# Optimization experiments

Measured on AMD Instinct MI355X. Metric: run time of the kernel, lower is better.

## Reference

```python
import jax, jax.numpy as jnp
import numpy as np

H = 512
S = 65  # 64 board cells + appended constant 1


def _heads(y, wk, wq, wv):
    # y: [H, S]; wk/wq/wv: [3, H, H] -> atts: [3, S, H]
    def one(wk_i, wq_i, wv_i):
        k = wk_i @ y            # [H, S]
        q = wq_i @ y            # [H, S]
        v = wv_i @ y            # [H, S]
        sm = jax.nn.softmax(k.T @ q, axis=1)  # [S, S], softmax over dim=1
        return sm @ v.T         # [S, H]
    return jax.vmap(one)(wk, wq, wv)


def setup_inputs() -> dict:
    key = jax.random.key(0)
    ks = jax.random.split(key, 10)
    r = lambda k, s: jax.random.normal(k, s, dtype=jnp.float32)
    return {
        "inputs": r(ks[0], (1, 64)),
        "embedding": r(ks[1], (H, S)),
        "wq": r(ks[2], (3, 3, H, H)),
        "wk": r(ks[3], (3, 3, H, H)),
        "wv": r(ks[4], (3, 3, H, H)),
        "linear1": r(ks[5], (3 * H, H)),
        "linear2": r(ks[6], (3 * H, H)),
        "linear3": r(ks[7], (3 * H, 2 * H)),
        "linear4": r(ks[8], (2 * H, H)),
        "linear5": r(ks[9], (H, 64)),
    }


def reference(inputs, embedding, wq, wk, wv, linear1, linear2, linear3, linear4, linear5):
    x = jnp.concatenate([inputs[0], jnp.ones((1,), inputs.dtype)])  # [S]
    y = embedding * x  # [H, S] (broadcast over rows)

    # Layer 1 (3 heads)
    a1 = _heads(y, wk[0], wq[0], wv[0])  # [3, S, H]
    y = jax.nn.relu(jnp.concatenate([a1[0], a1[1], a1[2]], axis=1) @ linear1).T  # [H, S]

    # Layer 2 -- NOTE: original code cats att11, att12, att23 (a bug we preserve)
    a2 = _heads(y, wk[1], wq[1], wv[1])
    y = jax.nn.relu(jnp.concatenate([a1[0], a1[1], a2[2]], axis=1) @ linear2).T  # [H, S]

    # Layer 3 -- NOTE: original code cats att11, att12, att33 (preserved)
    a3 = _heads(y, wk[2], wq[2], wv[2])
    y = jax.nn.relu(jnp.concatenate([a1[0], a1[1], a3[2]], axis=1) @ linear3)[64]  # [2H]

    # dropout p=0.1 -> identity in eval mode
    y = jnp.tanh(y @ linear4)  # [H]
    score = y @ linear5        # [64]
    return score[None, :]      # [1, 64]
```

## Files before the change

kernel.cpp:

```cpp
#include <hip/hip_runtime.h>
#include <hip/hip_bf16.h>
#include <math.h>

#define H 512
#define S 65
#define SP 80
#define HS (H * S)
#define PHS (H * SP)
#define KS3 24
#define KS4 16


__global__ void scale_embed_kernel(const float* __restrict__ inp,
                                   const float* __restrict__ emb,
                                   float* __restrict__ yT) {
    int i = blockIdx.x * blockDim.x + threadIdx.x;
    if (i < PHS) {
        int s = i / H;
        int h = i % H;
        float v = 0.0f;
        if (s < S) {
            float x = (s == 64) ? 1.0f : inp[s];
            v = emb[h * S + s] * x;
        }
        yT[i] = v;
    }
}

__global__ void __launch_bounds__(256, 2)
kqv_gemm_tiled(const float* __restrict__ wq,
               const float* __restrict__ wk,
               const float* __restrict__ wv,
               int layer, int head0,
               const float* __restrict__ yT,
               float* __restrict__ part) {
    int slot  = blockIdx.z;
    int which = blockIdx.y;
    int mat = layer * 3 + head0 + slot;
    const float* W = (which == 0 ? wk : (which == 1 ? wq : wv)) + (size_t)mat * H * H;

    int n0   = (blockIdx.x & 7) * 64;
    int kidx = blockIdx.x >> 3;

    __shared__ float Wt[64 * 64];
    __shared__ float As[SP * 64];

    int t  = threadIdx.x;
    int nq = t & 15;
    int g  = t >> 4;

    float4 acc[5];
#pragma unroll
    for (int r = 0; r < 5; ++r) acc[r] = make_float4(0.f, 0.f, 0.f, 0.f);

    for (int ch = 0; ch < 4; ++ch) {
        int kc0 = kidx * 256 + ch * 64;

#pragma unroll
        for (int c = 0; c < 4; ++c) {
            int f = c * 256 + t;
            int wn  = f >> 4;
            int kf4 = f & 15;
            float4 w4 = *(const float4*)(W + (size_t)(n0 + wn) * H + kc0 + 4 * kf4);
            int sw = ((wn >> 2) ^ (kf4 & 7));
            int base = (4 * kf4) * 64 + 4 * sw + (wn & 3);
            Wt[base      ] = w4.x;
            Wt[base +  64] = w4.y;
            Wt[base + 128] = w4.z;
            Wt[base + 192] = w4.w;
        }
#pragma unroll
        for (int c = 0; c < 5; ++c) {
            int f = c * 256 + t;
            int as  = f >> 4;
            int kf4 = f & 15;
            *(float4*)(&As[as * 64 + 4 * kf4]) =
                *(const float4*)(yT + (size_t)as * H + kc0 + 4 * kf4);
        }
        __syncthreads();

#pragma unroll
        for (int k4 = 0; k4 < 16; ++k4) {
            int swc = 4 * (nq ^ (k4 & 7));
            float4 w0 = *(const float4*)(&Wt[(4 * k4 + 0) * 64 + swc]);
            float4 w1 = *(const float4*)(&Wt[(4 * k4 + 1) * 64 + swc]);
            float4 w2 = *(const float4*)(&Wt[(4 * k4 + 2) * 64 + swc]);
            float4 w3 = *(const float4*)(&Wt[(4 * k4 + 3) * 64 + swc]);
#pragma unroll
            for (int r = 0; r < 5; ++r) {
                float4 a = *(const float4*)(&As[(g + 16 * r) * 64 + 4 * k4]);
                acc[r].x = fmaf(a.x, w0.x, acc[r].x);
                acc[r].y = fmaf(a.x, w0.y, acc[r].y);
                acc[r].z = fmaf(a.x, w0.z, acc[r].z);
                acc[r].w = fmaf(a.x, w0.w, acc[r].w);
                acc[r].x = fmaf(a.y, w1.x, acc[r].x);
                acc[r].y = fmaf(a.y, w1.y, acc[r].y);
                acc[r].z = fmaf(a.y, w1.z, acc[r].z);
                acc[r].w = fmaf(a.y, w1.w, acc[r].w);
                acc[r].x = fmaf(a.z, w2.x, acc[r].x);
                acc[r].y = fmaf(a.z, w2.y, acc[r].y);
                acc[r].z = fmaf(a.z, w2.z, acc[r].z);
                acc[r].w = fmaf(a.z, w2.w, acc[r].w);
                acc[r].x = fmaf(a.w, w3.x, acc[r].x);
                acc[r].y = fmaf(a.w, w3.y, acc[r].y);
                acc[r].z = fmaf(a.w, w3.z, acc[r].z);
                acc[r].w = fmaf(a.w, w3.w, acc[r].w);
            }
        }
        __syncthreads();
    }

    float* P = part + (size_t)((slot * 3 + which) * 2 + kidx) * PHS;
#pragma unroll
    for (int r = 0; r < 5; ++r) {
        *(float4*)(P + (size_t)(g + 16 * r) * H + n0 + 4 * nq) = acc[r];
    }
}

__global__ void kqv_combine_kernel(const float* __restrict__ part,
                                   float* __restrict__ kT,
                                   float* __restrict__ qT,
                                   float* __restrict__ vT) {
    int slot  = blockIdx.z;
    int which = blockIdx.y;
    int i = blockIdx.x * 256 + threadIdx.x;
    float* out = (which == 0 ? kT : (which == 1 ? qT : vT)) + (size_t)slot * PHS;
    const float* P = part + (size_t)((slot * 3 + which) * 2) * PHS;
    out[i] = P[i] + P[PHS + i];
}

__global__ void attn_kernel(const float* __restrict__ kT,
                            const float* __restrict__ qT,
                            const float* __restrict__ vT,
                            float* __restrict__ att, int a_offset) {
    int a = blockIdx.x + a_offset;
    int slot = blockIdx.y;
    int tid = threadIdx.x;

    const float* kk = kT + (size_t)slot * PHS;
    const float* qq = qT + (size_t)slot * PHS;
    const float* vv = vT + (size_t)slot * PHS;
    float* ao = att + (size_t)slot * S * H;

    __shared__ float sm[S];
    __shared__ float p[S];

    const float4* ka = (const float4*)(kk + (size_t)a * H);
    for (int b = tid; b < S; b += 64) {
        const float4* qb = (const float4*)(qq + (size_t)b * H);
        float4 c0 = {0,0,0,0}, c1 = {0,0,0,0}, c2 = {0,0,0,0}, c3 = {0,0,0,0};
        for (int t = 0; t < H / 4; t += 4) {
            float4 k0 = ka[t+0], k1 = ka[t+1], k2 = ka[t+2], k3 = ka[t+3];
            float4 q0 = qb[t+0], q1 = qb[t+1], q2 = qb[t+2], q3 = qb[t+3];
            c0.x = fmaf(k0.x, q0.x, c0.x); c0.y = fmaf(k0.y, q0.y, c0.y);
            c0.z = fmaf(k0.z, q0.z, c0.z); c0.w = fmaf(k0.w, q0.w, c0.w);
            c1.x = fmaf(k1.x, q1.x, c1.x); c1.y = fmaf(k1.y, q1.y, c1.y);
            c1.z = fmaf(k1.z, q1.z, c1.z); c1.w = fmaf(k1.w, q1.w, c1.w);
            c2.x = fmaf(k2.x, q2.x, c2.x); c2.y = fmaf(k2.y, q2.y, c2.y);
            c2.z = fmaf(k2.z, q2.z, c2.z); c2.w = fmaf(k2.w, q2.w, c2.w);
            c3.x = fmaf(k3.x, q3.x, c3.x); c3.y = fmaf(k3.y, q3.y, c3.y);
            c3.z = fmaf(k3.z, q3.z, c3.z); c3.w = fmaf(k3.w, q3.w, c3.w);
        }
        sm[b] = ((c0.x + c0.y) + (c0.z + c0.w)) + ((c1.x + c1.y) + (c1.z + c1.w))
              + ((c2.x + c2.y) + (c2.z + c2.w)) + ((c3.x + c3.y) + (c3.z + c3.w));
    }
    __syncthreads();

    float maxv = -INFINITY;
    for (int i = 0; i < S; ++i) maxv = fmaxf(maxv, sm[i]);
    float sum = 0.0f;
    for (int i = 0; i < S; ++i) sum += expf(sm[i] - maxv);
    float inv = 1.0f / sum;
    for (int b = tid; b < S; b += 64) {
        p[b] = expf(sm[b] - maxv) * inv;
    }
    __syncthreads();

    for (int hh = tid; hh < H; hh += 64) {
        float a0 = 0.f, a1 = 0.f, a2 = 0.f, a3 = 0.f;
        for (int b = 0; b < 64; b += 4) {
            a0 = fmaf(p[b + 0], vv[(b + 0) * H + hh], a0);
            a1 = fmaf(p[b + 1], vv[(b + 1) * H + hh], a1);
            a2 = fmaf(p[b + 2], vv[(b + 2) * H + hh], a2);
            a3 = fmaf(p[b + 3], vv[(b + 3) * H + hh], a3);
        }
        a0 = fmaf(p[64], vv[64 * H + hh], a0);
        ao[(size_t)a * H + hh] = (a0 + a1) + (a2 + a3);
    }
}

__global__ void linear_partial_kernel(const float* __restrict__ attA,
                                      const float* __restrict__ attB,
                                      const float* __restrict__ attC,
                                      const float* __restrict__ lin,
                                      float* __restrict__ part) {
    int seg = blockIdx.y;
    const float* att = (seg < 2) ? attA : (seg < 4 ? attB : attC);
    int i = blockIdx.x * blockDim.x + threadIdx.x;
    if (i >= HS) return;
    int s = i / H;
    int h = i % H;

    const float* row = att + (size_t)s * H + (seg & 1) * 256;
    const float* L = lin + (size_t)(seg * 256) * H + h;

    float a0 = 0.f, a1 = 0.f, a2 = 0.f, a3 = 0.f;
    for (int j = 0; j < 256; j += 4) {
        a0 = fmaf(row[j + 0], L[(size_t)(j + 0) * H], a0);
        a1 = fmaf(row[j + 1], L[(size_t)(j + 1) * H], a1);
        a2 = fmaf(row[j + 2], L[(size_t)(j + 2) * H], a2);
        a3 = fmaf(row[j + 3], L[(size_t)(j + 3) * H], a3);
    }
    part[(size_t)seg * HS + i] = (a0 + a1) + (a2 + a3);
}

__global__ void combine_relu_kernel(const float* __restrict__ part,
                                    float* __restrict__ yT) {
    int i = blockIdx.x * blockDim.x + threadIdx.x;
    if (i >= HS) return;
    float s = part[i] + part[HS + i] + part[2 * HS + i]
            + part[3 * HS + i] + part[4 * HS + i] + part[5 * HS + i];
    yT[i] = fmaxf(s, 0.0f);
}

__global__ void lin3_partial_kernel(const float* __restrict__ attA,
                                    const float* __restrict__ attB,
                                    const float* __restrict__ attC,
                                    const float* __restrict__ lin3,
                                    float* __restrict__ tpart) {
    int j2 = blockIdx.x * 256 + threadIdx.x;
    int ks = blockIdx.y;
    const float* row = (ks < 8) ? (attA + (size_t)64 * H)
                     : (ks < 16 ? (attB + (size_t)64 * H)
                                : (attC + (size_t)64 * H));
    int j0 = (ks & 7) * 64;
    int jbase = ks * 64;

    float a0 = 0.f, a1 = 0.f, a2 = 0.f, a3 = 0.f;
    for (int j = 0; j < 64; j += 4) {
        a0 = fmaf(row[j0 + j + 0], lin3[(size_t)(jbase + j + 0) * 1024 + j2], a0);
        a1 = fmaf(row[j0 + j + 1], lin3[(size_t)(jbase + j + 1) * 1024 + j2], a1);
        a2 = fmaf(row[j0 + j + 2], lin3[(size_t)(jbase + j + 2) * 1024 + j2], a2);
        a3 = fmaf(row[j0 + j + 3], lin3[(size_t)(jbase + j + 3) * 1024 + j2], a3);
    }
    tpart[ks * 1024 + j2] = (a0 + a1) + (a2 + a3);
}

__global__ void lin4_partial_kernel(const float* __restrict__ tpart,
                                    const float* __restrict__ lin4,
                                    float* __restrict__ upart) {
    __shared__ float tl[64];
    int hh = blockIdx.x * 256 + threadIdx.x;
    int ks = blockIdx.y;
    int j2base = ks * 64;

    if (threadIdx.x < 64) {
        int j2 = j2base + threadIdx.x;
        float s = 0.f;
#pragma unroll
        for (int p = 0; p < KS3; ++p) s += tpart[p * 1024 + j2];
        tl[threadIdx.x] = fmaxf(s, 0.f);
    }
    __syncthreads();

    float a0 = 0.f, a1 = 0.f, a2 = 0.f, a3 = 0.f;
    for (int j = 0; j < 64; j += 4) {
        a0 = fmaf(tl[j + 0], lin4[(size_t)(j2base + j + 0) * H + hh], a0);
        a1 = fmaf(tl[j + 1], lin4[(size_t)(j2base + j + 1) * H + hh], a1);
        a2 = fmaf(tl[j + 2], lin4[(size_t)(j2base + j + 2) * H + hh], a2);
        a3 = fmaf(tl[j + 3], lin4[(size_t)(j2base + j + 3) * H + hh], a3);
    }
    upart[ks * H + hh] = (a0 + a1) + (a2 + a3);
}

__global__ void final_out_kernel(const float* __restrict__ upart,
                                 const float* __restrict__ lin5,
                                 float* __restrict__ out) {
    __shared__ float u[H];
    __shared__ float pr[8][64];
    int tid = threadIdx.x;

    {
        float s = 0.f;
#pragma unroll
        for (int p = 0; p < KS4; ++p) s += upart[p * H + tid];
        u[tid] = tanhf(s);
    }
    __syncthreads();

    int o  = tid & 63;
    int sl = tid >> 6;
    float acc = 0.f;
    int h0 = sl * 64;
#pragma unroll 8
    for (int j = 0; j < 64; ++j) {
        acc = fmaf(u[h0 + j], lin5[(h0 + j) * 64 + o], acc);
    }
    pr[sl][o] = acc;
    __syncthreads();

    if (tid < 64) {
        float s = 0.f;
#pragma unroll
        for (int p = 0; p < 8; ++p) s += pr[p][tid];
        out[tid] = s;
    }
}

extern "C" void kernel_launch(void* const* d_in, const int* in_sizes, int n_in,
                              void* d_out, int out_size, void* d_ws, size_t ws_size,
                              hipStream_t stream) {
    const float* inputs  = (const float*)d_in[0];
    const float* emb     = (const float*)d_in[1];
    const float* wq      = (const float*)d_in[2];
    const float* wk      = (const float*)d_in[3];
    const float* wv      = (const float*)d_in[4];
    const float* linear1 = (const float*)d_in[5];
    const float* linear2 = (const float*)d_in[6];
    const float* linear3 = (const float*)d_in[7];
    const float* linear4 = (const float*)d_in[8];
    const float* linear5 = (const float*)d_in[9];
    float* out = (float*)d_out;

    float* ws    = (float*)d_ws;
    float* y     = ws;
    float* kT    = y     + PHS;
    float* qT    = kT    + 3 * PHS;
    float* vT    = qT    + 3 * PHS;
    float* att1  = vT    + 3 * PHS;
    float* att2  = att1  + 3 * HS;
    float* att3  = att2  + HS;
    float* part  = att3  + HS;
    float* tpart = part  + 6 * HS;
    float* upart = tpart + KS3 * 1024;
    float* kqvp  = upart + KS4 * H;

    const int nb  = HS / 256;
    const int nbp = PHS / 256;

    scale_embed_kernel<<<nbp, 256, 0, stream>>>(inputs, emb, y);

    kqv_gemm_tiled<<<dim3(16, 3, 3), 256, 0, stream>>>(wq, wk, wv, 0, 0, y, kqvp);
    kqv_combine_kernel<<<dim3(nbp, 3, 3), 256, 0, stream>>>(kqvp, kT, qT, vT);
    attn_kernel<<<dim3(S, 3), 64, 0, stream>>>(kT, qT, vT, att1, 0);
    linear_partial_kernel<<<dim3(nb, 6), 256, 0, stream>>>(att1, att1 + HS, att1 + 2 * HS,
                                                           linear1, part);
    combine_relu_kernel<<<nb, 256, 0, stream>>>(part, y);

    kqv_gemm_tiled<<<dim3(16, 3, 1), 256, 0, stream>>>(wq, wk, wv, 1, 2, y, kqvp);
    kqv_combine_kernel<<<dim3(nbp, 3, 1), 256, 0, stream>>>(kqvp, kT, qT, vT);
    attn_kernel<<<dim3(S, 1), 64, 0, stream>>>(kT, qT, vT, att2, 0);
    linear_partial_kernel<<<dim3(nb, 6), 256, 0, stream>>>(att1, att1 + HS, att2,
                                                           linear2, part);
    combine_relu_kernel<<<nb, 256, 0, stream>>>(part, y);

    kqv_gemm_tiled<<<dim3(16, 3, 1), 256, 0, stream>>>(wq, wk, wv, 2, 2, y, kqvp);
    kqv_combine_kernel<<<dim3(nbp, 3, 1), 256, 0, stream>>>(kqvp, kT, qT, vT);
    attn_kernel<<<dim3(1, 1), 64, 0, stream>>>(kT, qT, vT, att3, 64);

    lin3_partial_kernel<<<dim3(4, KS3), 256, 0, stream>>>(att1, att1 + HS, att3, linear3, tpart);
    lin4_partial_kernel<<<dim3(2, KS4), 256, 0, stream>>>(tpart, linear4, upart);
    final_out_kernel<<<1, 512, 0, stream>>>(upart, linear5, out);
}
```

Measured before the change: 264.5 us.

## Fuse split-K combine into attention and hoist layer-1-only linear partials early

Removes the kqv_combine kernels by summing the two split-K partials directly inside the attention kernels, and widens the attention block to 256 threads. Linear1, the att1-dependent parts of linear2, and the att1 part of linear3 are now computed right after layer-1 attention in larger batched launches, leaving only the att2 segment for layer 2. Layer-3 attention for row 64 is fused with its linear3 segment. This cuts launch count and intermediate traffic, at the cost of redundant attention recomputation across the 32 fused blocks and extra partial-buffer workspace.

```diff
diff --git a/kernel.cpp b/kernel.cpp
--- a/kernel.cpp
+++ b/kernel.cpp
@@ -117,92 +117,96 @@
     }
 }
 
-__global__ void kqv_combine_kernel(const float* __restrict__ part,
-                                   float* __restrict__ kT,
-                                   float* __restrict__ qT,
-                                   float* __restrict__ vT) {
-    int slot  = blockIdx.z;
-    int which = blockIdx.y;
-    int i = blockIdx.x * 256 + threadIdx.x;
-    float* out = (which == 0 ? kT : (which == 1 ? qT : vT)) + (size_t)slot * PHS;
-    const float* P = part + (size_t)((slot * 3 + which) * 2) * PHS;
-    out[i] = P[i] + P[PHS + i];
-}
-
-__global__ void attn_kernel(const float* __restrict__ kT,
-                            const float* __restrict__ qT,
-                            const float* __restrict__ vT,
-                            float* __restrict__ att, int a_offset) {
-    int a = blockIdx.x + a_offset;
+__global__ void attn_kernel(const float* __restrict__ kqvp,
+                            float* __restrict__ att) {
+    int a = blockIdx.x;
     int slot = blockIdx.y;
     int tid = threadIdx.x;
 
-    const float* kk = kT + (size_t)slot * PHS;
-    const float* qq = qT + (size_t)slot * PHS;
-    const float* vv = vT + (size_t)slot * PHS;
+    const float* K0 = kqvp + (size_t)(slot * 3 + 0) * 2 * PHS;
+    const float* K1 = K0 + PHS;
+    const float* Q0 = kqvp + (size_t)(slot * 3 + 1) * 2 * PHS;
+    const float* Q1 = Q0 + PHS;
+    const float* V0 = kqvp + (size_t)(slot * 3 + 2) * 2 * PHS;
+    const float* V1 = V0 + PHS;
     float* ao = att + (size_t)slot * S * H;
 
-    __shared__ float sm[S];
+    __shared__ float ka[H];
+    __shared__ float smv[S];
     __shared__ float p[S];
 
-    const float4* ka = (const float4*)(kk + (size_t)a * H);
-    for (int b = tid; b < S; b += 64) {
-        const float4* qb = (const float4*)(qq + (size_t)b * H);
-        float4 c0 = {0,0,0,0}, c1 = {0,0,0,0}, c2 = {0,0,0,0}, c3 = {0,0,0,0};
-        for (int t = 0; t < H / 4; t += 4) {
-            float4 k0 = ka[t+0], k1 = ka[t+1], k2 = ka[t+2], k3 = ka[t+3];
-            float4 q0 = qb[t+0], q1 = qb[t+1], q2 = qb[t+2], q3 = qb[t+3];
-            c0.x = fmaf(k0.x, q0.x, c0.x); c0.y = fmaf(k0.y, q0.y, c0.y);
-            c0.z = fmaf(k0.z, q0.z, c0.z); c0.w = fmaf(k0.w, q0.w, c0.w);
-            c1.x = fmaf(k1.x, q1.x, c1.x); c1.y = fmaf(k1.y, q1.y, c1.y);
-            c1.z = fmaf(k1.z, q1.z, c1.z); c1.w = fmaf(k1.w, q1.w, c1.w);
-            c2.x = fmaf(k2.x, q2.x, c2.x); c2.y = fmaf(k2.y, q2.y, c2.y);
-            c2.z = fmaf(k2.z, q2.z, c2.z); c2.w = fmaf(k2.w, q2.w, c2.w);
-            c3.x = fmaf(k3.x, q3.x, c3.x); c3.y = fmaf(k3.y, q3.y, c3.y);
-            c3.z = fmaf(k3.z, q3.z, c3.z); c3.w = fmaf(k3.w, q3.w, c3.w);
-        }
-        sm[b] = ((c0.x + c0.y) + (c0.z + c0.w)) + ((c1.x + c1.y) + (c1.z + c1.w))
-              + ((c2.x + c2.y) + (c2.z + c2.w)) + ((c3.x + c3.y) + (c3.z + c3.w));
+    ka[tid]       = K0[(size_t)a * H + tid]       + K1[(size_t)a * H + tid];
+    ka[tid + 256] = K0[(size_t)a * H + tid + 256] + K1[(size_t)a * H + tid + 256];
+    __syncthreads();
+
+    if (tid < S) {
+        const float4* q0 = (const float4*)(Q0 + (size_t)tid * H);
+        const float4* q1 = (const float4*)(Q1 + (size_t)tid * H);
+        const float4* kl = (const float4*)ka;
+        float4 c0 = {0,0,0,0}, c1 = {0,0,0,0};
+        for (int t = 0; t < H / 4; t += 2) {
+            float4 qa = q0[t],     qb = q1[t];
+            float4 qc = q0[t + 1], qd = q1[t + 1];
+            float4 k0 = kl[t], k1 = kl[t + 1];
+            c0.x = fmaf(k0.x, qa.x + qb.x, c0.x);
+            c0.y = fmaf(k0.y, qa.y + qb.y, c0.y);
+            c0.z = fmaf(k0.z, qa.z + qb.z, c0.z);
+            c0.w = fmaf(k0.w, qa.w + qb.w, c0.w);
+            c1.x = fmaf(k1.x, qc.x + qd.x, c1.x);
+            c1.y = fmaf(k1.y, qc.y + qd.y, c1.y);
+            c1.z = fmaf(k1.z, qc.z + qd.z, c1.z);
+            c1.w = fmaf(k1.w, qc.w + qd.w, c1.w);
+        }
+        smv[tid] = ((c0.x + c0.y) + (c0.z + c0.w)) + ((c1.x + c1.y) + (c1.z + c1.w));
     }
     __syncthreads();
 
     float maxv = -INFINITY;
-    for (int i = 0; i < S; ++i) maxv = fmaxf(maxv, sm[i]);
+    for (int i = 0; i < S; ++i) maxv = fmaxf(maxv, smv[i]);
     float sum = 0.0f;
-    for (int i = 0; i < S; ++i) sum += expf(sm[i] - maxv);
+    for (int i = 0; i < S; ++i) sum += expf(smv[i] - maxv);
     float inv = 1.0f / sum;
-    for (int b = tid; b < S; b += 64) {
-        p[b] = expf(sm[b] - maxv) * inv;
-    }
-    __syncthreads();
-
-    for (int hh = tid; hh < H; hh += 64) {
-        float a0 = 0.f, a1 = 0.f, a2 = 0.f, a3 = 0.f;
-        for (int b = 0; b < 64; b += 4) {
-            a0 = fmaf(p[b + 0], vv[(b + 0) * H + hh], a0);
-            a1 = fmaf(p[b + 1], vv[(b + 1) * H + hh], a1);
-            a2 = fmaf(p[b + 2], vv[(b + 2) * H + hh], a2);
-            a3 = fmaf(p[b + 3], vv[(b + 3) * H + hh], a3);
-        }
-        a0 = fmaf(p[64], vv[64 * H + hh], a0);
-        ao[(size_t)a * H + hh] = (a0 + a1) + (a2 + a3);
-    }
-}
-
-__global__ void linear_partial_kernel(const float* __restrict__ attA,
-                                      const float* __restrict__ attB,
-                                      const float* __restrict__ attC,
-                                      const float* __restrict__ lin,
-                                      float* __restrict__ part) {
+    if (tid < S) p[tid] = expf(smv[tid] - maxv) * inv;
+    __syncthreads();
+
+#pragma unroll
+    for (int rep = 0; rep < 2; ++rep) {
+        int hh = tid + rep * 256;
+        float a0 = 0.f, a1 = 0.f;
+#pragma unroll 4
+        for (int b = 0; b < 64; b += 2) {
+            a0 = fmaf(p[b    ], V0[(size_t)(b    ) * H + hh] + V1[(size_t)(b    ) * H + hh], a0);
+            a1 = fmaf(p[b + 1], V0[(size_t)(b + 1) * H + hh] + V1[(size_t)(b + 1) * H + hh], a1);
+        }
+        a0 = fmaf(p[64], V0[(size_t)64 * H + hh] + V1[(size_t)64 * H + hh], a0);
+        ao[(size_t)a * H + hh] = a0 + a1;
+    }
+}
+
+__global__ void linA_kernel(const float* __restrict__ att1,
+                            const float* __restrict__ lin1,
+                            const float* __restrict__ lin2,
+                            float* __restrict__ part1,
+                            float* __restrict__ part2) {
     int seg = blockIdx.y;
-    const float* att = (seg < 2) ? attA : (seg < 4 ? attB : attC);
     int i = blockIdx.x * blockDim.x + threadIdx.x;
-    if (i >= HS) return;
     int s = i / H;
     int h = i % H;
 
+    const float* att;
+    const float* L;
+    float* dst;
+    if (seg < 6) {
+        att = att1 + (size_t)(seg >> 1) * HS;
+        L   = lin1 + (size_t)(seg * 256) * H + h;
+        dst = part1 + (size_t)seg * HS;
+    } else {
+        int s2 = seg - 6;
+        att = att1 + (size_t)(s2 >> 1) * HS;
+        L   = lin2 + (size_t)(s2 * 256) * H + h;
+        dst = part2 + (size_t)s2 * HS;
+    }
     const float* row = att + (size_t)s * H + (seg & 1) * 256;
-    const float* L = lin + (size_t)(seg * 256) * H + h;
 
     float a0 = 0.f, a1 = 0.f, a2 = 0.f, a3 = 0.f;
     for (int j = 0; j < 256; j += 4) {
@@ -211,7 +215,28 @@
         a2 = fmaf(row[j + 2], L[(size_t)(j + 2) * H], a2);
         a3 = fmaf(row[j + 3], L[(size_t)(j + 3) * H], a3);
     }
-    part[(size_t)seg * HS + i] = (a0 + a1) + (a2 + a3);
+    dst[i] = (a0 + a1) + (a2 + a3);
+}
+
+__global__ void lin2c_kernel(const float* __restrict__ att2,
+                             const float* __restrict__ lin2,
+                             float* __restrict__ part2) {
+    int seg = 4 + blockIdx.y;
+    int i = blockIdx.x * blockDim.x + threadIdx.x;
+    int s = i / H;
+    int h = i % H;
+
+    const float* row = att2 + (size_t)s * H + (seg & 1) * 256;
+    const float* L = lin2 + (size_t)(seg * 256) * H + h;
+
+    float a0 = 0.f, a1 = 0.f, a2 = 0.f, a3 = 0.f;
+    for (int j = 0; j < 256; j += 4) {
+        a0 = fmaf(row[j + 0], L[(size_t)(j + 0) * H], a0);
+        a1 = fmaf(row[j + 1], L[(size_t)(j + 1) * H], a1);
+        a2 = fmaf(row[j + 2], L[(size_t)(j + 2) * H], a2);
+        a3 = fmaf(row[j + 3], L[(size_t)(j + 3) * H], a3);
+    }
+    part2[(size_t)seg * HS + i] = (a0 + a1) + (a2 + a3);
 }
 
 __global__ void combine_relu_kernel(const float* __restrict__ part,
@@ -223,16 +248,12 @@
     yT[i] = fmaxf(s, 0.0f);
 }
 
-__global__ void lin3_partial_kernel(const float* __restrict__ attA,
-                                    const float* __restrict__ attB,
-                                    const float* __restrict__ attC,
-                                    const float* __restrict__ lin3,
-                                    float* __restrict__ tpart) {
+__global__ void lin3ab_kernel(const float* __restrict__ att1,
+                              const float* __restrict__ lin3,
+                              float* __restrict__ tpart) {
     int j2 = blockIdx.x * 256 + threadIdx.x;
     int ks = blockIdx.y;
-    const float* row = (ks < 8) ? (attA + (size_t)64 * H)
-                     : (ks < 16 ? (attB + (size_t)64 * H)
-                                : (attC + (size_t)64 * H));
+    const float* row = att1 + (size_t)(ks >> 3) * HS + (size_t)64 * H;
     int j0 = (ks & 7) * 64;
     int jbase = ks * 64;
 
@@ -242,6 +263,84 @@
         a1 = fmaf(row[j0 + j + 1], lin3[(size_t)(jbase + j + 1) * 1024 + j2], a1);
         a2 = fmaf(row[j0 + j + 2], lin3[(size_t)(jbase + j + 2) * 1024 + j2], a2);
         a3 = fmaf(row[j0 + j + 3], lin3[(size_t)(jbase + j + 3) * 1024 + j2], a3);
+    }
+    tpart[ks * 1024 + j2] = (a0 + a1) + (a2 + a3);
+}
+
+__global__ void attn3_lin3c_kernel(const float* __restrict__ kqvp,
+                                   const float* __restrict__ lin3,
+                                   float* __restrict__ tpart) {
+    int tid = threadIdx.x;
+    int ks  = 16 + blockIdx.y;
+    int j2  = blockIdx.x * 256 + tid;
+    int j0  = (ks & 7) * 64;
+
+    const float* K0 = kqvp;
+    const float* K1 = kqvp + PHS;
+    const float* Q0 = kqvp + 2 * (size_t)PHS;
+    const float* Q1 = kqvp + 3 * (size_t)PHS;
+    const float* V0 = kqvp + 4 * (size_t)PHS;
+    const float* V1 = kqvp + 5 * (size_t)PHS;
+
+    __shared__ float ka[H];
+    __shared__ float smv[S];
+    __shared__ float p[S];
+    __shared__ float att_s[64];
+
+    ka[tid]       = K0[(size_t)64 * H + tid]       + K1[(size_t)64 * H + tid];
+    ka[tid + 256] = K0[(size_t)64 * H + tid + 256] + K1[(size_t)64 * H + tid + 256];
+    __syncthreads();
+
+    if (tid < S) {
+        const float4* q0 = (const float4*)(Q0 + (size_t)tid * H);
+        const float4* q1 = (const float4*)(Q1 + (size_t)tid * H);
+        const float4* kl = (const float4*)ka;
+        float4 c0 = {0,0,0,0}, c1 = {0,0,0,0};
+        for (int t = 0; t < H / 4; t += 2) {
+            float4 qa = q0[t],     qb = q1[t];
+            float4 qc = q0[t + 1], qd = q1[t + 1];
+            float4 k0 = kl[t], k1 = kl[t + 1];
+            c0.x = fmaf(k0.x, qa.x + qb.x, c0.x);
+            c0.y = fmaf(k0.y, qa.y + qb.y, c0.y);
+            c0.z = fmaf(k0.z, qa.z + qb.z, c0.z);
+            c0.w = fmaf(k0.w, qa.w + qb.w, c0.w);
+            c1.x = fmaf(k1.x, qc.x + qd.x, c1.x);
+            c1.y = fmaf(k1.y, qc.y + qd.y, c1.y);
+            c1.z = fmaf(k1.z, qc.z + qd.z, c1.z);
+            c1.w = fmaf(k1.w, qc.w + qd.w, c1.w);
+        }
+        smv[tid] = ((c0.x + c0.y) + (c0.z + c0.w)) + ((c1.x + c1.y) + (c1.z + c1.w));
+    }
+    __syncthreads();
+
+    float maxv = -INFINITY;
+    for (int i = 0; i < S; ++i) maxv = fmaxf(maxv, smv[i]);
+    float sum = 0.0f;
+    for (int i = 0; i < S; ++i) sum += expf(smv[i] - maxv);
+    float inv = 1.0f / sum;
+    if (tid < S) p[tid] = expf(smv[tid] - maxv) * inv;
+    __syncthreads();
+
+    if (tid < 64) {
+        int hh = j0 + tid;
+        float a0 = 0.f, a1 = 0.f;
+#pragma unroll 4
+        for (int b = 0; b < 64; b += 2) {
+            a0 = fmaf(p[b    ], V0[(size_t)(b    ) * H + hh] + V1[(size_t)(b    ) * H + hh], a0);
+            a1 = fmaf(p[b + 1], V0[(size_t)(b + 1) * H + hh] + V1[(size_t)(b + 1) * H + hh], a1);
+        }
+        a0 = fmaf(p[64], V0[(size_t)64 * H + hh] + V1[(size_t)64 * H + hh], a0);
+        att_s[tid] = a0 + a1;
+    }
+    __syncthreads();
+
+    int jbase = ks * 64;
+    float a0 = 0.f, a1 = 0.f, a2 = 0.f, a3 = 0.f;
+    for (int j = 0; j < 64; j += 4) {
+        a0 = fmaf(att_s[j + 0], lin3[(size_t)(jbase + j + 0) * 1024 + j2], a0);
+        a1 = fmaf(att_s[j + 1], lin3[(size_t)(jbase + j + 1) * 1024 + j2], a1);
+        a2 = fmaf(att_s[j + 2], lin3[(size_t)(jbase + j + 2) * 1024 + j2], a2);
+        a3 = fmaf(att_s[j + 3], lin3[(size_t)(jbase + j + 3) * 1024 + j2], a3);
     }
     tpart[ks * 1024 + j2] = (a0 + a1) + (a2 + a3);
 }
@@ -324,16 +423,13 @@
 
     float* ws    = (float*)d_ws;
     float* y     = ws;
-    float* kT    = y     + PHS;
-    float* qT    = kT    + 3 * PHS;
-    float* vT    = qT    + 3 * PHS;
-    float* att1  = vT    + 3 * PHS;
+    float* kqvp  = y     + PHS;
+    float* att1  = kqvp  + 18 * PHS;
     float* att2  = att1  + 3 * HS;
-    float* att3  = att2  + HS;
-    float* part  = att3  + HS;
-    float* tpart = part  + 6 * HS;
+    float* part1 = att2  + HS;
+    float* part2 = part1 + 6 * HS;
+    float* tpart = part2 + 6 * HS;
     float* upart = tpart + KS3 * 1024;
-    float* kqvp  = upart + KS4 * H;
 
     const int nb  = HS / 256;
     const int nbp = PHS / 256;
@@ -341,24 +437,19 @@
     scale_embed_kernel<<<nbp, 256, 0, stream>>>(inputs, emb, y);
 
     kqv_gemm_tiled<<<dim3(16, 3, 3), 256, 0, stream>>>(wq, wk, wv, 0, 0, y, kqvp);
-    kqv_combine_kernel<<<dim3(nbp, 3, 3), 256, 0, stream>>>(kqvp, kT, qT, vT);
-    attn_kernel<<<dim3(S, 3), 64, 0, stream>>>(kT, qT, vT, att1, 0);
-    linear_partial_kernel<<<dim3(nb, 6), 256, 0, stream>>>(att1, att1 + HS, att1 + 2 * HS,
-                                                           linear1, part);
-    combine_relu_kernel<<<nb, 256, 0, stream>>>(part, y);
+    attn_kernel<<<dim3(S, 3), 256, 0, stream>>>(kqvp, att1);
+    linA_kernel<<<dim3(nb, 10), 256, 0, stream>>>(att1, linear1, linear2, part1, part2);
+    lin3ab_kernel<<<dim3(4, 16), 256, 0, stream>>>(att1, linear3, tpart);
+    combine_relu_kernel<<<nb, 256, 0, stream>>>(part1, y);
 
     kqv_gemm_tiled<<<dim3(16, 3, 1), 256, 0, stream>>>(wq, wk, wv, 1, 2, y, kqvp);
-    kqv_combine_kernel<<<dim3(nbp, 3, 1), 256, 0, stream>>>(kqvp, kT, qT, vT);
-    attn_kernel<<<dim3(S, 1), 64, 0, stream>>>(kT, qT, vT, att2, 0);
-    linear_partial_kernel<<<dim3(nb, 6), 256, 0, stream>>>(att1, att1 + HS, att2,
-                                                           linear2, part);
-    combine_relu_kernel<<<nb, 256, 0, stream>>>(part, y);
+    attn_kernel<<<dim3(S, 1), 256, 0, stream>>>(kqvp, att2);
+    lin2c_kernel<<<dim3(nb, 2), 256, 0, stream>>>(att2, linear2, part2);
+    combine_relu_kernel<<<nb, 256, 0, stream>>>(part2, y);
 
     kqv_gemm_tiled<<<dim3(16, 3, 1), 256, 0, stream>>>(wq, wk, wv, 2, 2, y, kqvp);
-    kqv_combine_kernel<<<dim3(nbp, 3, 1), 256, 0, stream>>>(kqvp, kT, qT, vT);
-    attn_kernel<<<dim3(1, 1), 64, 0, stream>>>(kT, qT, vT, att3, 64);
-
-    lin3_partial_kernel<<<dim3(4, KS3), 256, 0, stream>>>(att1, att1 + HS, att3, linear3, tpart);
+    attn3_lin3c_kernel<<<dim3(4, 8), 256, 0, stream>>>(kqvp, linear3, tpart);
+
     lin4_partial_kernel<<<dim3(2, KS4), 256, 0, stream>>>(tpart, linear4, upart);
     final_out_kernel<<<1, 512, 0, stream>>>(upart, linear5, out);
 }
```

Measured after the change: 262.2 us. Within noise of the previous version (-0.8%).
